# Kernel optimization log

Hardware: AMD Instinct MI355X
Metric: run time of the kernel (lower is better)

## Reference

```python
import jax, jax.numpy as jnp
import numpy as np

N = 50000      # nodes
E = 800000     # edges (avg degree 16)
F_IN = 32      # raw node feature dim
H = 96         # hidden_channels == encoder.output_dim (skip_connection=True)
EDGE_DIM = 16
L = 3          # num_layers
B = 50         # graphs in batch
MSG_IN = 2 * H + 1 + EDGE_DIM   # [h_i, h_j, ||dpos||^2, edge_attr]
NODE_IN = 2 * H                 # [h_i, aggregated message]


def setup_inputs() -> dict:
    key = jax.random.key(0)
    ks = jax.random.split(key, 14)

    def w(k, shape):
        fan_in = shape[-2]
        return jax.random.normal(k, shape, jnp.float32) * (1.0 / np.sqrt(fan_in))

    return {
        "x": jax.random.normal(ks[0], (N, F_IN), jnp.float32),
        "pos": jax.random.normal(ks[1], (N, 3), jnp.float32),
        "edge_index": jax.random.randint(ks[2], (2, E), 0, N),
        "edge_attr": jax.random.normal(ks[3], (E, EDGE_DIM), jnp.float32),
        "batch_indices": jnp.sort(jax.random.randint(ks[4], (N,), 0, B)),
        # encoder (modeled as a linear projection to H)
        "We": w(ks[5], (F_IN, H)), "be": jnp.zeros((H,), jnp.float32),
        # per-layer EGNN edge MLP: Linear(MSG_IN,H)-SiLU-Linear(H,H)-SiLU
        "eW1": w(ks[6], (L, MSG_IN, H)), "eb1": jnp.zeros((L, H), jnp.float32),
        "eW2": w(ks[7], (L, H, H)), "eb2": jnp.zeros((L, H), jnp.float32),
        # per-layer EGNN node MLP: Linear(NODE_IN,H)-SiLU-Linear(H,H)
        "nW1": w(ks[8], (L, NODE_IN, H)), "nb1": jnp.zeros((L, H), jnp.float32),
        "nW2": w(ks[9], (L, H, H)), "nb2": jnp.zeros((L, H), jnp.float32),
        "Wl": w(ks[10], (H, 1)), "bl": jnp.zeros((1,), jnp.float32),
    }


def reference(x, pos, edge_index, edge_attr, batch_indices,
              We, be, eW1, eb1, eW2, eb2, nW1, nb1, nW2, nb2, Wl, bl):
    silu = jax.nn.silu
    src, dst = edge_index[0], edge_index[1]

    # encoder: project raw features to hidden dim
    h = x @ We + be                                    # [N, H]

    # squared pairwise distances along edges (pos fixed, update_pos=False)
    rel = pos[src] - pos[dst]                          # [E, 3]
    d2 = jnp.sum(rel * rel, axis=-1, keepdims=True)    # [E, 1]

    for l in range(L):
        feat = jnp.concatenate([h[src], h[dst], d2, edge_attr], axis=-1)  # [E, MSG_IN]
        m = silu(silu(feat @ eW1[l] + eb1[l]) @ eW2[l] + eb2[l])          # [E, H]
        agg = jax.ops.segment_sum(m, dst, num_segments=N)                 # [N, H]
        upd = silu(jnp.concatenate([h, agg], axis=-1) @ nW1[l] + nb1[l]) @ nW2[l] + nb2[l]
        h = h + upd  # skip_connection=True

    # global_mean_pool over graphs
    counts = jax.ops.segment_sum(jnp.ones((N, 1), h.dtype), batch_indices, num_segments=B)
    pooled = jax.ops.segment_sum(h, batch_indices, num_segments=B) / jnp.maximum(counts, 1.0)

    return pooled @ Wl + bl                            # [B, 1]
```

## Files before the change

kernel.cpp:

```cpp
#include <hip/hip_runtime.h>

#define Nn 50000
#define Ee 800000
#define FIN 32
#define EDIM 16
#define Bb 50
#define NTILES 12500
#define TPX 1563

typedef _Float16 half8 __attribute__((ext_vector_type(8)));
typedef float floatx4 __attribute__((ext_vector_type(4)));

#define OFF_WeT 0
#define WT_LAYER(l) (3072 + (l) * 58368)
#define OFF_W1AB 0
#define OFF_W1C  18432
#define OFF_W2   21504
#define OFF_NW1  30720
#define OFF_NW2  49152
#define WT_TOTAL 178176

__device__ __forceinline__ float silu_f(float x) {
    return __fdividef(x, 1.0f + __expf(-x));
}

__device__ __forceinline__ int lower_bound_i(const int* a, int n, int v) {
    int lo = 0, hi = n;
    while (lo < hi) { int m = (lo + hi) >> 1; if (a[m] < v) lo = m + 1; else hi = m; }
    return lo;
}

__device__ __forceinline__ half8 ldg_h8(const _Float16* p) {
    return *(const half8*)p;
}

__device__ __forceinline__ half8 h8_zero() {
    half8 z;
    #pragma unroll
    for (int j = 0; j < 8; j++) z[j] = (_Float16)0.f;
    return z;
}

__global__ void k_prepw(const float* __restrict__ We, const float* __restrict__ eW1,
                        const float* __restrict__ eW2, const float* __restrict__ nW1,
                        const float* __restrict__ nW2, _Float16* __restrict__ wT) {
    int idx = blockIdx.x * 256 + threadIdx.x;
    if (idx >= WT_TOTAL) return;
    float v;
    if (idx < 3072) {
        int n = idx >> 5, k = idx & 31;
        v = We[k * 96 + n];
    } else {
        int j = idx - 3072;
        int l = j / 58368, r = j % 58368;
        const float* eW1l = eW1 + l * 209 * 96;
        if (r < 18432) {
            int n = r / 96, k = r % 96;
            v = (n < 96) ? eW1l[k * 96 + n] : eW1l[(96 + k) * 96 + (n - 96)];
        } else if (r < 21504) {
            int r2 = r - 18432;
            int n = r2 >> 5, k = r2 & 31;
            v = (k < 16) ? eW1l[(193 + k) * 96 + n]
              : (k == 16) ? eW1l[192 * 96 + n] : 0.f;
        } else if (r < 30720) {
            int r2 = r - 21504;
            int n = r2 / 96, k = r2 % 96;
            v = eW2[l * 9216 + k * 96 + n];
        } else if (r < 49152) {
            int r2 = r - 30720;
            int n = r2 / 192, k = r2 % 192;
            v = nW1[l * 18432 + k * 96 + n];
        } else {
            int r2 = r - 49152;
            int n = r2 / 96, k = r2 % 96;
            v = nW2[l * 9216 + k * 96 + n];
        }
    }
    wT[idx] = (_Float16)v;
}

__global__ void k_prep(const int* __restrict__ ei, const float* __restrict__ pos,
                       float* __restrict__ d2, int* __restrict__ counts) {
    int e = blockIdx.x * 256 + threadIdx.x;
    if (e >= Ee) return;
    int s = ei[e], d = ei[Ee + e];
    float dx = pos[s * 3 + 0] - pos[d * 3 + 0];
    float dy = pos[s * 3 + 1] - pos[d * 3 + 1];
    float dz = pos[s * 3 + 2] - pos[d * 3 + 2];
    d2[e] = dx * dx + dy * dy + dz * dz;
    atomicAdd(&counts[d], 1);
}

__global__ void k_scanA(const int* __restrict__ counts, int* __restrict__ rowstart,
                        int* __restrict__ bsums) {
    __shared__ int s[256];
    int b = blockIdx.x, t = threadIdx.x, i = b * 256 + t;
    int v = (i < Nn) ? counts[i] : 0;
    s[t] = v;
    __syncthreads();
    for (int off = 1; off < 256; off <<= 1) {
        int add = (t >= off) ? s[t - off] : 0;
        __syncthreads();
        s[t] += add;
        __syncthreads();
    }
    if (i < Nn) rowstart[i + 1] = s[t];
    if (t == 255) bsums[b] = s[255];
}

__global__ void k_scanB(int* __restrict__ bsums, int nb) {
    __shared__ int s[256];
    int t = threadIdx.x;
    int v = (t < nb) ? bsums[t] : 0;
    s[t] = v;
    __syncthreads();
    for (int off = 1; off < 256; off <<= 1) {
        int add = (t >= off) ? s[t - off] : 0;
        __syncthreads();
        s[t] += add;
        __syncthreads();
    }
    if (t < nb) bsums[t] = s[t] - v;
}

__global__ void k_scanC(int* __restrict__ rowstart, const int* __restrict__ bsums) {
    int b = blockIdx.x, t = threadIdx.x, i = b * 256 + t;
    if (i < Nn) rowstart[i + 1] += bsums[b];
    if (i == 0 && b == 0) rowstart[0] = 0;
}

__global__ void k_fill(const int* __restrict__ ei, const float* __restrict__ ea,
                       const float* __restrict__ d2, const int* __restrict__ rowstart,
                       int* __restrict__ cur, int* __restrict__ srcs_p,
                       int* __restrict__ dsts_p, _Float16* __restrict__ eap16,
                       _Float16* __restrict__ d2h) {
    int e = blockIdx.x * 256 + threadIdx.x;
    if (e >= Ee) return;
    int s = ei[e], d = ei[Ee + e];
    int slot = rowstart[d] + atomicAdd(&cur[d], 1);
    srcs_p[slot] = s;
    dsts_p[slot] = d;
    const float4* ea4 = (const float4*)ea;
    float4 q0 = ea4[e * 4 + 0], q1 = ea4[e * 4 + 1];
    float4 q2 = ea4[e * 4 + 2], q3 = ea4[e * 4 + 3];
    half8 c0, c1;
    c0[0]=(_Float16)q0.x; c0[1]=(_Float16)q0.y; c0[2]=(_Float16)q0.z; c0[3]=(_Float16)q0.w;
    c0[4]=(_Float16)q1.x; c0[5]=(_Float16)q1.y; c0[6]=(_Float16)q1.z; c0[7]=(_Float16)q1.w;
    c1[0]=(_Float16)q2.x; c1[1]=(_Float16)q2.y; c1[2]=(_Float16)q2.z; c1[3]=(_Float16)q2.w;
    c1[4]=(_Float16)q3.x; c1[5]=(_Float16)q3.y; c1[6]=(_Float16)q3.z; c1[7]=(_Float16)q3.w;
    half8* dst8 = (half8*)(eap16 + (size_t)slot * 16);
    dst8[0] = c0; dst8[1] = c1;
    d2h[slot] = (_Float16)d2[e];
}

__global__ __launch_bounds__(256, 4)
void k_encab(const float* __restrict__ x, const _Float16* __restrict__ WeT,
             const float* __restrict__ be, const _Float16* __restrict__ W1abT,
             _Float16* __restrict__ h16, _Float16* __restrict__ A16,
             _Float16* __restrict__ B16, float* __restrict__ agg) {
    __shared__ _Float16 x16[64][40];
    __shared__ _Float16 hs[64][104];
    int t = threadIdx.x;
    int n0 = blockIdx.x * 64;
    for (int i = t; i < 64 * 32; i += 256) {
        int nl = i >> 5, k = i & 31;
        int n = n0 + nl;
        x16[nl][k] = (_Float16)((n < Nn) ? x[n * FIN + k] : 0.f);
    }
    __syncthreads();
    int lane = t & 63, quad = lane >> 4, lm = lane & 15, w = t >> 6;
    half8 af = *(const half8*)&x16[w * 16 + lm][quad * 8];
    for (int nt = 0; nt < 6; nt++) {
        int col = nt * 16 + lm;
        float b = be[col];
        floatx4 acc = {b, b, b, b};
        half8 bf = ldg_h8(WeT + col * 32 + quad * 8);
        acc = __builtin_amdgcn_mfma_f32_16x16x32_f16(af, bf, acc, 0, 0, 0);
        #pragma unroll
        for (int r = 0; r < 4; r++)
            hs[w * 16 + quad * 4 + r][col] = (_Float16)acc[r];
    }
    __syncthreads();
    #pragma unroll
    for (int i = 0; i < 3; i++) {
        int ci = t + 256 * i;
        int el = ci / 12, c0 = (ci % 12) * 8;
        int n = n0 + el;
        if (n < Nn) *(half8*)(h16 + n * 96 + c0) = *(half8*)&hs[el][c0];
    }
    for (int i = t; i < 64 * 24; i += 256) {
        int el = i / 24, c = (i % 24) * 4;
        int n = n0 + el;
        if (n < Nn) *(float4*)(agg + n * 96 + c) = make_float4(0.f, 0.f, 0.f, 0.f);
    }
    half8 af3[3];
    #pragma unroll
    for (int kt = 0; kt < 3; kt++)
        af3[kt] = *(const half8*)&hs[w * 16 + lm][kt * 32 + quad * 8];
    for (int nt = 0; nt < 12; nt++) {
        int col = nt * 16 + lm;
        floatx4 acc = {0.f, 0.f, 0.f, 0.f};
        #pragma unroll
        for (int kt = 0; kt < 3; kt++) {
            half8 bf = ldg_h8(W1abT + col * 96 + kt * 32 + quad * 8);
            acc = __builtin_amdgcn_mfma_f32_16x16x32_f16(af3[kt], bf, acc, 0, 0, 0);
        }
        #pragma unroll
        for (int r = 0; r < 4; r++) {
            int n = n0 + w * 16 + quad * 4 + r;
            if (n < Nn) {
                if (col < 96) A16[n * 96 + col] = (_Float16)acc[r];
                else          B16[n * 96 + col - 96] = (_Float16)acc[r];
            }
        }
    }
}

__global__ __launch_bounds__(256, 4)
void k_edge(const _Float16* __restrict__ A16, const _Float16* __restrict__ B16,
            const _Float16* __restrict__ eap16, const _Float16* __restrict__ d2h,
            const int* __restrict__ srcs_p, const int* __restrict__ dsts_p,
            const _Float16* __restrict__ W1cT, const float* __restrict__ eb1l,
            const _Float16* __restrict__ W2T, const float* __restrict__ eb2l,
            float* __restrict__ agg) {
    __shared__ _Float16 u16[64][104];
    __shared__ _Float16 W2f[18 * 64 * 8];
    __shared__ _Float16 W1f[6 * 64 * 8];
    __shared__ int srcs_s[64], dsts_s[64];

    int t = threadIdx.x;
    int lane = t & 63, quad = lane >> 4, lm = lane & 15, w = t >> 6;

    for (int f = w; f < 18; f += 4) {
        int nt = f / 3, kt = f % 3;
        half8 v = ldg_h8(W2T + (nt * 16 + lm) * 96 + kt * 32 + quad * 8);
        *(half8*)&W2f[(f * 64 + lane) * 8] = v;
    }
    for (int f = w; f < 6; f += 4) {
        half8 v = ldg_h8(W1cT + (f * 16 + lm) * 32 + quad * 8);
        *(half8*)&W1f[(f * 64 + lane) * 8] = v;
    }

    float eb1v[6], eb2v[6];
    #pragma unroll
    for (int nt = 0; nt < 6; nt++) {
        eb1v[nt] = eb1l[nt * 16 + lm];
        eb2v[nt] = eb2l[nt * 16 + lm];
    }
    __syncthreads();

    int xcd = blockIdx.x & 7, ib = blockIdx.x >> 3;
    int nbx = gridDim.x >> 3;
    for (int k = ib; k < TPX; k += nbx) {
        int tile = xcd * TPX + k;
        if (tile >= NTILES) break;
        int e0 = tile * 64;
        int sv = 0, dv = 0;
        if (t < 64) { sv = srcs_p[e0 + t]; dv = dsts_p[e0 + t]; }
        int erow = e0 + w * 16 + lm;
        half8 af1;
        if (quad == 0)      af1 = ldg_h8(eap16 + (size_t)erow * 16);
        else if (quad == 1) af1 = ldg_h8(eap16 + (size_t)erow * 16 + 8);
        else { af1 = h8_zero(); if (quad == 2) af1[0] = d2h[erow]; }
        __syncthreads();
        if (t < 64) { srcs_s[t] = sv; dsts_s[t] = dv; }
        for (int nt = 0; nt < 6; nt++) {
            floatx4 acc = {eb1v[nt], eb1v[nt], eb1v[nt], eb1v[nt]};
            half8 bf = *(const half8*)&W1f[(nt * 64 + lane) * 8];
            acc = __builtin_amdgcn_mfma_f32_16x16x32_f16(af1, bf, acc, 0, 0, 0);
            #pragma unroll
            for (int r = 0; r < 4; r++)
                u16[w * 16 + quad * 4 + r][nt * 16 + lm] = (_Float16)acc[r];
        }
        __syncthreads();
        #pragma unroll
        for (int i = 0; i < 3; i++) {
            int ci = t + 256 * i;
            int el = ci / 12, c0 = (ci % 12) * 8;
            half8 av = ldg_h8(A16 + srcs_s[el] * 96 + c0);
            half8 bv = ldg_h8(B16 + dsts_s[el] * 96 + c0);
            half8 pv = *(half8*)&u16[el][c0];
            half8 res;
            #pragma unroll
            for (int j = 0; j < 8; j++)
                res[j] = (_Float16)silu_f((float)pv[j] + (float)av[j] + (float)bv[j]);
            *(half8*)&u16[el][c0] = res;
        }
        __syncthreads();
        half8 af2[3];
        #pragma unroll
        for (int kt = 0; kt < 3; kt++)
            af2[kt] = *(const half8*)&u16[w * 16 + lm][kt * 32 + quad * 8];
        for (int nt = 0; nt < 6; nt++) {
            floatx4 acc = {eb2v[nt], eb2v[nt], eb2v[nt], eb2v[nt]};
            #pragma unroll
            for (int kt = 0; kt < 3; kt++) {
                half8 bf = *(const half8*)&W2f[((nt * 3 + kt) * 64 + lane) * 8];
                acc = __builtin_amdgcn_mfma_f32_16x16x32_f16(af2[kt], bf, acc, 0, 0, 0);
            }
            #pragma unroll
            for (int r = 0; r < 4; r++)
                u16[w * 16 + quad * 4 + r][nt * 16 + lm] = (_Float16)silu_f(acc[r]);
        }
        __syncthreads();
        if (t < 192) {
            int j = t % 96, half_ = t / 96;
            int eb_ = half_ * 32, ee_ = eb_ + 32;
            float run = 0.f;
            int cd = dsts_s[eb_];
            for (int e = eb_; e < ee_; e++) {
                int dn = dsts_s[e];
                if (dn != cd) { atomicAdd(&agg[cd * 96 + j], run); run = 0.f; cd = dn; }
                run += (float)u16[e][j];
            }
            atomicAdd(&agg[cd * 96 + j], run);
        }
    }
}

__global__ __launch_bounds__(256, 4)
void k_nodeab(_Float16* __restrict__ h16, float* __restrict__ agg,
              const _Float16* __restrict__ nW1T, const float* __restrict__ nb1l,
              const _Float16* __restrict__ nW2T, const float* __restrict__ nb2l,
              const _Float16* __restrict__ W1abT, _Float16* __restrict__ A16,
              _Float16* __restrict__ B16, int do_ab) {
    __shared__ _Float16 in16[64][200];
    __shared__ _Float16 t116[64][104];
    int t = threadIdx.x, n0 = blockIdx.x * 64;
    #pragma unroll
    for (int i = 0; i < 3; i++) {
        int ci = t + 256 * i;
        int el = ci / 12, c0 = (ci % 12) * 8;
        int n = n0 + el;
        half8 hv = h8_zero();
        half8 av = h8_zero();
        if (n < Nn) {
            hv = ldg_h8(h16 + n * 96 + c0);
            float4 a = *(const float4*)(agg + n * 96 + c0);
            float4 b = *(const float4*)(agg + n * 96 + c0 + 4);
            av[0]=(_Float16)a.x; av[1]=(_Float16)a.y; av[2]=(_Float16)a.z; av[3]=(_Float16)a.w;
            av[4]=(_Float16)b.x; av[5]=(_Float16)b.y; av[6]=(_Float16)b.z; av[7]=(_Float16)b.w;
        }
        *(half8*)&in16[el][c0] = hv;
        *(half8*)&in16[el][96 + c0] = av;
    }
    __syncthreads();
    int lane = t & 63, quad = lane >> 4, lm = lane & 15, w = t >> 6;
    half8 af[6];
    #pragma unroll
    for (int kt = 0; kt < 6; kt++)
        af[kt] = *(const half8*)&in16[w * 16 + lm][kt * 32 + quad * 8];
    for (int nt = 0; nt < 6; nt++) {
        int col = nt * 16 + lm;
        float b = nb1l[col];
        floatx4 acc = {b, b, b, b};
        #pragma unroll
        for (int kt = 0; kt < 6; kt++) {
            half8 bf = ldg_h8(nW1T + col * 192 + kt * 32 + quad * 8);
            acc = __builtin_amdgcn_mfma_f32_16x16x32_f16(af[kt], bf, acc, 0, 0, 0);
        }
        #pragma unroll
        for (int r = 0; r < 4; r++)
            t116[w * 16 + quad * 4 + r][col] = (_Float16)silu_f(acc[r]);
    }
    __syncthreads();
    half8 af2[3];
    #pragma unroll
    for (int kt = 0; kt < 3; kt++)
        af2[kt] = *(const half8*)&t116[w * 16 + lm][kt * 32 + quad * 8];
    __syncthreads();
    for (int nt = 0; nt < 6; nt++) {
        int col = nt * 16 + lm;
        float b = nb2l[col];
        floatx4 acc = {b, b, b, b};
        #pragma unroll
        for (int kt = 0; kt < 3; kt++) {
            half8 bf = ldg_h8(nW2T + col * 96 + kt * 32 + quad * 8);
            acc = __builtin_amdgcn_mfma_f32_16x16x32_f16(af2[kt], bf, acc, 0, 0, 0);
        }
        #pragma unroll
        for (int r = 0; r < 4; r++) {
            int row = w * 16 + quad * 4 + r;
            float hnew = (float)in16[row][col] + acc[r];
            in16[row][col] = (_Float16)hnew;
        }
    }
    __syncthreads();
    #pragma unroll
    for (int i = 0; i < 3; i++) {
        int ci = t + 256 * i;
        int el = ci / 12, c0 = (ci % 12) * 8;
        int n = n0 + el;
        if (n < Nn) *(half8*)(h16 + n * 96 + c0) = *(half8*)&in16[el][c0];
    }
    if (!do_ab) return;
    half8 af3[3];
    #pragma unroll
    for (int kt = 0; kt < 3; kt++)
        af3[kt] = *(const half8*)&in16[w * 16 + lm][kt * 32 + quad * 8];
    for (int nt = 0; nt < 12; nt++) {
        int col = nt * 16 + lm;
        floatx4 acc = {0.f, 0.f, 0.f, 0.f};
        #pragma unroll
        for (int kt = 0; kt < 3; kt++) {
            half8 bf = ldg_h8(W1abT + col * 96 + kt * 32 + quad * 8);
            acc = __builtin_amdgcn_mfma_f32_16x16x32_f16(af3[kt], bf, acc, 0, 0, 0);
        }
        #pragma unroll
        for (int r = 0; r < 4; r++) {
            int n = n0 + w * 16 + quad * 4 + r;
            if (n < Nn) {
                if (col < 96) A16[n * 96 + col] = (_Float16)acc[r];
                else          B16[n * 96 + col - 96] = (_Float16)acc[r];
            }
        }
    }
    for (int i = t; i < 64 * 24; i += 256) {
        int el = i / 24, c = (i % 24) * 4;
        int n = n0 + el;
        if (n < Nn) *(float4*)(agg + n * 96 + c) = make_float4(0.f, 0.f, 0.f, 0.f);
    }
}

__global__ void k_pool_partial(const _Float16* __restrict__ h16, const int* __restrict__ batch,
                               float* __restrict__ pooled) {
    int g = blockIdx.x >> 2, q = blockIdx.x & 3;
    int start = lower_bound_i(batch, Nn, g);
    int end   = lower_bound_i(batch, Nn, g + 1);
    int len = end - start;
    int chunk = (len + 3) >> 2;
    int s = start + q * chunk;
    int e = min(s + chunk, end);
    int t = threadIdx.x;
    int j = t % 96, r = t / 96;
    float sum = 0.f;
    for (int n = s + r; n < e; n += 2) sum += (float)h16[n * 96 + j];
    atomicAdd(&pooled[g * 96 + j], sum);
}

__global__ void k_final(const float* __restrict__ pooled, const int* __restrict__ batch,
                        const float* __restrict__ Wl, const float* __restrict__ bl,
                        float* __restrict__ out) {
    int g = blockIdx.x, lane = threadIdx.x;
    int start = lower_bound_i(batch, Nn, g);
    int end   = lower_bound_i(batch, Nn, g + 1);
    int cnt = end - start; if (cnt < 1) cnt = 1;
    float v = 0.f;
    for (int j = lane; j < 96; j += 64) v += pooled[g * 96 + j] * Wl[j];
    #pragma unroll
    for (int off = 32; off > 0; off >>= 1) v += __shfl_down(v, off);
    if (lane == 0) out[g] = v / (float)cnt + bl[0];
}

extern "C" void kernel_launch(void* const* d_in, const int* in_sizes, int n_in,
                              void* d_out, int out_size, void* d_ws, size_t ws_size,
                              hipStream_t stream) {
    const float* x     = (const float*)d_in[0];
    const float* pos   = (const float*)d_in[1];
    const int*   ei    = (const int*)d_in[2];
    const float* ea    = (const float*)d_in[3];
    const int*   batch = (const int*)d_in[4];
    const float* We    = (const float*)d_in[5];
    const float* be    = (const float*)d_in[6];
    const float* eW1   = (const float*)d_in[7];
    const float* eb1   = (const float*)d_in[8];
    const float* eW2   = (const float*)d_in[9];
    const float* eb2   = (const float*)d_in[10];
    const float* nW1   = (const float*)d_in[11];
    const float* nb1   = (const float*)d_in[12];
    const float* nW2   = (const float*)d_in[13];
    const float* nb2   = (const float*)d_in[14];
    const float* Wl    = (const float*)d_in[15];
    const float* bl    = (const float*)d_in[16];
    float* out = (float*)d_out;

    float* ws = (float*)d_ws;
    _Float16* h16    = (_Float16*)(ws);
    _Float16* A16    = (_Float16*)(ws + 2400000);
    _Float16* B16    = (_Float16*)(ws + 4800000);
    float*    agg    = ws + 7200000;
    float*    d2     = ws + 12000000;
    float*    pooled = ws + 12800000;
    int*      counts   = (int*)(ws + 12804800);
    int*      cur      = (int*)(ws + 12854800);
    int*      rowstart = (int*)(ws + 12904800);
    int*      bsums    = (int*)(ws + 12954816);
    int*      srcs_p   = (int*)(ws + 12955072);
    int*      dsts_p   = (int*)(ws + 13755072);
    _Float16* eap16    = (_Float16*)(ws + 14555072);
    _Float16* d2h      = (_Float16*)(ws + 20955072);
    _Float16* wT       = (_Float16*)(ws + 21355072);

    hipMemsetAsync(counts, 0, 2 * 50000 * sizeof(int), stream);
    hipMemsetAsync(pooled, 0, Bb * 96 * sizeof(float), stream);

    k_prepw<<<dim3(696), dim3(256), 0, stream>>>(We, eW1, eW2, nW1, nW2, wT);
    k_prep<<<dim3(3125), dim3(256), 0, stream>>>(ei, pos, d2, counts);
    k_scanA<<<dim3(196), dim3(256), 0, stream>>>(counts, rowstart, bsums);
    k_scanB<<<dim3(1), dim3(256), 0, stream>>>(bsums, 196);
    k_scanC<<<dim3(196), dim3(256), 0, stream>>>(rowstart, bsums);
    k_fill<<<dim3(3125), dim3(256), 0, stream>>>(ei, ea, d2, rowstart, cur,
                                                 srcs_p, dsts_p, eap16, d2h);
    k_encab<<<dim3(782), dim3(256), 0, stream>>>(x, wT + OFF_WeT, be,
        wT + WT_LAYER(0) + OFF_W1AB, h16, A16, B16, agg);

    for (int l = 0; l < 3; l++) {
        const _Float16* wl = wT + WT_LAYER(l);
        k_edge<<<dim3(1024), dim3(256), 0, stream>>>(A16, B16, eap16, d2h,
            srcs_p, dsts_p, wl + OFF_W1C, eb1 + l * 96, wl + OFF_W2, eb2 + l * 96, agg);
        const _Float16* wnext = wT + WT_LAYER(l < 2 ? l + 1 : 0);
        k_nodeab<<<dim3(782), dim3(256), 0, stream>>>(h16, agg,
            wl + OFF_NW1, nb1 + l * 96, wl + OFF_NW2, nb2 + l * 96,
            wnext + OFF_W1AB, A16, B16, (l < 2) ? 1 : 0);
    }
    k_pool_partial<<<dim3(200), dim3(192), 0, stream>>>(h16, batch, pooled);
    k_final<<<dim3(50), dim3(64), 0, stream>>>(pooled, batch, Wl, bl, out);
}
```

Before: 761.0 us.

## Make edge-kernel tiles wave-independent and drop block barriers

The edge kernel now gives each wave its own independent 16-edge slot instead of a 64-edge block tile. This removes all __syncthreads and the shared src/dst index arrays. Each lane gathers A/B node rows directly in the MFMA output layout and fuses the add with SiLU in registers. Aggregation becomes a register-level segmented reduction: a ballot fast path issues one atomic per column when all 16 edges share a destination, otherwise runs are flushed per 4-edge group. The trade-off is more scalar, less coalesced gathers, potentially more atomics, and a hardcoded 512-slot stride that assumes a particular grid size.

```diff
diff --git a/kernel.cpp b/kernel.cpp
--- a/kernel.cpp
+++ b/kernel.cpp
@@ -5,8 +5,7 @@
 #define FIN 32
 #define EDIM 16
 #define Bb 50
-#define NTILES 12500
-#define TPX 1563
+#define SPX 6250
 
 typedef _Float16 half8 __attribute__((ext_vector_type(8)));
 typedef float floatx4 __attribute__((ext_vector_type(4)));
@@ -226,7 +225,6 @@
     __shared__ _Float16 u16[64][104];
     __shared__ _Float16 W2f[18 * 64 * 8];
     __shared__ _Float16 W1f[6 * 64 * 8];
-    __shared__ int srcs_s[64], dsts_s[64];
 
     int t = threadIdx.x;
     int lane = t & 63, quad = lane >> 4, lm = lane & 15, w = t >> 6;
@@ -240,7 +238,6 @@
         half8 v = ldg_h8(W1cT + (f * 16 + lm) * 32 + quad * 8);
         *(half8*)&W1f[(f * 64 + lane) * 8] = v;
     }
-
     float eb1v[6], eb2v[6];
     #pragma unroll
     for (int nt = 0; nt < 6; nt++) {
@@ -250,47 +247,38 @@
     __syncthreads();
 
     int xcd = blockIdx.x & 7, ib = blockIdx.x >> 3;
-    int nbx = gridDim.x >> 3;
-    for (int k = ib; k < TPX; k += nbx) {
-        int tile = xcd * TPX + k;
-        if (tile >= NTILES) break;
-        int e0 = tile * 64;
-        int sv = 0, dv = 0;
-        if (t < 64) { sv = srcs_p[e0 + t]; dv = dsts_p[e0 + t]; }
-        int erow = e0 + w * 16 + lm;
+    int slot = ib * 4 + w;
+    for (int s = slot; s < SPX; s += 512) {
+        int e0 = (xcd * SPX + s) * 16;
         half8 af1;
-        if (quad == 0)      af1 = ldg_h8(eap16 + (size_t)erow * 16);
-        else if (quad == 1) af1 = ldg_h8(eap16 + (size_t)erow * 16 + 8);
-        else { af1 = h8_zero(); if (quad == 2) af1[0] = d2h[erow]; }
-        __syncthreads();
-        if (t < 64) { srcs_s[t] = sv; dsts_s[t] = dv; }
+        if (quad == 0)      af1 = ldg_h8(eap16 + (size_t)(e0 + lm) * 16);
+        else if (quad == 1) af1 = ldg_h8(eap16 + (size_t)(e0 + lm) * 16 + 8);
+        else { af1 = h8_zero(); if (quad == 2) af1[0] = d2h[e0 + lm]; }
+        int sr[4], dr[4];
+        #pragma unroll
+        for (int r = 0; r < 4; r++) {
+            sr[r] = srcs_p[e0 + quad * 4 + r];
+            dr[r] = dsts_p[e0 + quad * 4 + r];
+        }
+        float m[6][4];
+        #pragma unroll
         for (int nt = 0; nt < 6; nt++) {
             floatx4 acc = {eb1v[nt], eb1v[nt], eb1v[nt], eb1v[nt]};
             half8 bf = *(const half8*)&W1f[(nt * 64 + lane) * 8];
             acc = __builtin_amdgcn_mfma_f32_16x16x32_f16(af1, bf, acc, 0, 0, 0);
             #pragma unroll
-            for (int r = 0; r < 4; r++)
-                u16[w * 16 + quad * 4 + r][nt * 16 + lm] = (_Float16)acc[r];
-        }
-        __syncthreads();
-        #pragma unroll
-        for (int i = 0; i < 3; i++) {
-            int ci = t + 256 * i;
-            int el = ci / 12, c0 = (ci % 12) * 8;
-            half8 av = ldg_h8(A16 + srcs_s[el] * 96 + c0);
-            half8 bv = ldg_h8(B16 + dsts_s[el] * 96 + c0);
-            half8 pv = *(half8*)&u16[el][c0];
-            half8 res;
-            #pragma unroll
-            for (int j = 0; j < 8; j++)
-                res[j] = (_Float16)silu_f((float)pv[j] + (float)av[j] + (float)bv[j]);
-            *(half8*)&u16[el][c0] = res;
-        }
-        __syncthreads();
+            for (int r = 0; r < 4; r++) {
+                float av = (float)A16[sr[r] * 96 + nt * 16 + lm];
+                float bv = (float)B16[dr[r] * 96 + nt * 16 + lm];
+                u16[w * 16 + quad * 4 + r][nt * 16 + lm] =
+                    (_Float16)silu_f(acc[r] + av + bv);
+            }
+        }
         half8 af2[3];
         #pragma unroll
         for (int kt = 0; kt < 3; kt++)
             af2[kt] = *(const half8*)&u16[w * 16 + lm][kt * 32 + quad * 8];
+        #pragma unroll
         for (int nt = 0; nt < 6; nt++) {
             floatx4 acc = {eb2v[nt], eb2v[nt], eb2v[nt], eb2v[nt]};
             #pragma unroll
@@ -299,21 +287,32 @@
                 acc = __builtin_amdgcn_mfma_f32_16x16x32_f16(af2[kt], bf, acc, 0, 0, 0);
             }
             #pragma unroll
-            for (int r = 0; r < 4; r++)
-                u16[w * 16 + quad * 4 + r][nt * 16 + lm] = (_Float16)silu_f(acc[r]);
-        }
-        __syncthreads();
-        if (t < 192) {
-            int j = t % 96, half_ = t / 96;
-            int eb_ = half_ * 32, ee_ = eb_ + 32;
-            float run = 0.f;
-            int cd = dsts_s[eb_];
-            for (int e = eb_; e < ee_; e++) {
-                int dn = dsts_s[e];
-                if (dn != cd) { atomicAdd(&agg[cd * 96 + j], run); run = 0.f; cd = dn; }
-                run += (float)u16[e][j];
+            for (int r = 0; r < 4; r++) m[nt][r] = silu_f(acc[r]);
+        }
+        bool eqloc = (dr[0] == dr[1]) && (dr[1] == dr[2]) && (dr[2] == dr[3]);
+        int dnext = __shfl_down(dr[0], 16);
+        bool cont = (lane >= 48) || (dr[3] == dnext);
+        unsigned long long mask = __ballot(eqloc && cont);
+        if (mask == ~0ULL) {
+            #pragma unroll
+            for (int nt = 0; nt < 6; nt++) {
+                float p = m[nt][0] + m[nt][1] + m[nt][2] + m[nt][3];
+                p += __shfl_xor(p, 16);
+                p += __shfl_xor(p, 32);
+                if (quad == 0) atomicAdd(&agg[dr[0] * 96 + nt * 16 + lm], p);
             }
-            atomicAdd(&agg[cd * 96 + j], run);
+        } else {
+            #pragma unroll
+            for (int nt = 0; nt < 6; nt++) {
+                int col = nt * 16 + lm;
+                float run = m[nt][0];
+                #pragma unroll
+                for (int r = 1; r < 4; r++) {
+                    if (dr[r] == dr[r - 1]) run += m[nt][r];
+                    else { atomicAdd(&agg[dr[r - 1] * 96 + col], run); run = m[nt][r]; }
+                }
+                atomicAdd(&agg[dr[3] * 96 + col], run);
+            }
         }
     }
 }
```

Measured after the change: 1.167 ms. 53.3% more time.
